# Performance work log

Measured on AMD Instinct MI355X. Metric: run time of the kernel, lower is better.

## Reference

```python
import jax, jax.numpy as jnp
import numpy as np

N_NODES = 100000
N_EDGES = 1600000
N_GRAPHS = 1024
N_FEAT = 128
HID = 64
N_CLASSES = 16
N_CENT = 3  # centroids per class


def setup_inputs() -> dict:
    key = jax.random.key(0)
    ks = jax.random.split(key, 8)
    x = jax.random.normal(ks[0], (N_NODES, N_FEAT), dtype=jnp.float32)
    edge_index = jax.random.randint(ks[1], (2, N_EDGES), 0, N_NODES, dtype=jnp.int64)
    batch = jnp.sort(jax.random.randint(ks[2], (N_NODES,), 0, N_GRAPHS, dtype=jnp.int64))
    s = 1.0 / np.sqrt(N_FEAT)
    W1 = jax.random.normal(ks[3], (N_FEAT, HID), dtype=jnp.float32) * s
    W2 = jax.random.normal(ks[4], (HID, HID), dtype=jnp.float32) * (1.0 / np.sqrt(HID))
    W3 = jax.random.normal(ks[5], (HID, HID), dtype=jnp.float32) * (1.0 / np.sqrt(HID))
    b1 = jnp.zeros((HID,), jnp.float32)
    b2 = jnp.zeros((HID,), jnp.float32)
    b3 = jnp.zeros((HID,), jnp.float32)
    centroids = jax.random.normal(ks[6], (N_CLASSES * N_CENT, HID), dtype=jnp.float32)
    reject_bias = jnp.zeros((1,), jnp.float32)
    return {"x": x, "edge_index": edge_index, "batch": batch,
            "W1": W1, "b1": b1, "W2": W2, "b2": b2, "W3": W3, "b3": b3,
            "centroids": centroids, "reject_bias": reject_bias}


def _gcn_conv(x, W, b, src, dst, norm, n_nodes):
    # PyG GCNConv: out[dst] = sum_e norm_e * (x[src_e] @ W), + bias
    h = x @ W                      # [N, out]
    msg = h[src] * norm[:, None]   # [E+N, out] gather + scale
    out = jax.ops.segment_sum(msg, dst, num_segments=n_nodes)
    return out + b


def reference(x, edge_index, batch, W1, b1, W2, b2, W3, b3, centroids, reject_bias):
    n = x.shape[0]
    loops = jnp.arange(n, dtype=edge_index.dtype)
    src = jnp.concatenate([edge_index[0], loops])
    dst = jnp.concatenate([edge_index[1], loops])
    # symmetric normalization on A + I
    deg = jax.ops.segment_sum(jnp.ones_like(dst, dtype=x.dtype), dst, num_segments=n)
    dinv = jax.lax.rsqrt(jnp.maximum(deg, 1.0))
    norm = dinv[src] * dinv[dst]

    h = jax.nn.relu(_gcn_conv(x, W1, b1, src, dst, norm, n))  # dropout is identity at eval
    h = jax.nn.relu(_gcn_conv(h, W2, b2, src, dst, norm, n))
    h = _gcn_conv(h, W3, b3, src, dst, norm, n)

    # global mean pool over graphs in the batch
    summ = jax.ops.segment_sum(h, batch, num_segments=N_GRAPHS)          # [G, HID]
    cnt = jax.ops.segment_sum(jnp.ones((n,), h.dtype), batch, num_segments=N_GRAPHS)
    emb = summ / jnp.maximum(cnt, 1.0)[:, None]

    # centroid distance head: squared euclidean to all class centroids
    d = (jnp.sum(emb * emb, -1, keepdims=True)
         - 2.0 * emb @ centroids.T
         + jnp.sum(centroids * centroids, -1))                           # [G, 16*3]
    d_pc = jnp.min(d.reshape(-1, N_CLASSES, N_CENT), axis=-1)            # [G, 16]
    class_logits = -d_pc
    reject_logit = jnp.min(d_pc, axis=-1, keepdims=True) - reject_bias   # [G, 1]
    return jnp.concatenate([class_logits, reject_logit], axis=-1)        # [G, 17]
```

## Files before the change

kernel.cpp:

```cpp
#include <hip/hip_runtime.h>

#define HID 64
#define NCLS 16
#define NCENT 3
#define NCENTS (NCLS * NCENT)
#define BSHIFT 9
#define BINW (1 << BSHIFT)
#define NBINMAX 256
#define CHUNK 4096
#define EPT (CHUNK / 256)
#define NU 8

static inline int ceil_div(int a, int b) { return (a + b - 1) / b; }

__device__ inline unsigned short f2bf(float f) {
    unsigned int u = __float_as_uint(f);
    return (unsigned short)((u + 0x7FFFu + ((u >> 16) & 1u)) >> 16);
}
__device__ inline unsigned int pack2bf(float lo, float hi) {
    return (unsigned int)f2bf(lo) | ((unsigned int)f2bf(hi) << 16);
}
__device__ inline float bf2f(unsigned short h) {
    return __uint_as_float(((unsigned int)h) << 16);
}
__device__ inline float bflo(unsigned int u) { return __uint_as_float(u << 16); }
__device__ inline float bfhi(unsigned int u) { return __uint_as_float(u & 0xFFFF0000u); }


__global__ void k_count(const int* __restrict__ dst, int* __restrict__ binCnt,
                        int E, int nbins) {
    __shared__ int c[NBINMAX];
    for (int i = threadIdx.x; i < nbins; i += 256) c[i] = 0;
    __syncthreads();
    int e = blockIdx.x * CHUNK + threadIdx.x;
#pragma unroll
    for (int j = 0; j < EPT; j++, e += 256)
        if (e < E) atomicAdd(&c[dst[e] >> BSHIFT], 1);
    __syncthreads();
    for (int i = threadIdx.x; i < nbins; i += 256)
        if (c[i] > 0) atomicAdd(&binCnt[i], c[i]);
}

__global__ void k_binoff(const int* __restrict__ binCnt, int* __restrict__ binBase,
                         int nbins, int E) {
    __shared__ int ts[NBINMAX];
    int t = threadIdx.x;
    int v = (t < nbins) ? binCnt[t] : 0;
    ts[t] = v;
    __syncthreads();
    for (int off = 1; off < NBINMAX; off <<= 1) {
        int x = (t >= off) ? ts[t - off] : 0;
        __syncthreads();
        ts[t] += x;
        __syncthreads();
    }
    if (t < nbins) binBase[t] = ts[t] - v;
    if (t == 0) binBase[nbins] = E;
}

__global__ __launch_bounds__(256) void k_bin(const int* __restrict__ src,
                                             const int* __restrict__ dst,
                                             const int* __restrict__ binBase,
                                             int* __restrict__ binCur,
                                             int2* __restrict__ binned,
                                             int E, int nbins) {
    __shared__ int cnt[NBINMAX], off[NBINMAX], gbase[NBINMAX];
    __shared__ int2 stage[CHUNK];
    const int c0 = blockIdx.x * CHUNK;
    const int tid = threadIdx.x;
    cnt[tid] = 0;
    __syncthreads();
    int sv[EPT], dv[EPT];
#pragma unroll
    for (int j = 0; j < EPT; j++) {
        int e = c0 + j * 256 + tid;
        dv[j] = -1;
        if (e < E) {
            sv[j] = src[e];
            dv[j] = dst[e];
            atomicAdd(&cnt[dv[j] >> BSHIFT], 1);
        }
    }
    __syncthreads();
    off[tid] = cnt[tid];
    __syncthreads();
    for (int o = 1; o < NBINMAX; o <<= 1) {
        int x = (tid >= o) ? off[tid - o] : 0;
        __syncthreads();
        off[tid] += x;
        __syncthreads();
    }
    int excl = off[tid] - cnt[tid];
    __syncthreads();
    off[tid] = excl;
    gbase[tid] = (tid < nbins && cnt[tid] > 0) ? atomicAdd(&binCur[tid], cnt[tid]) : 0;
    cnt[tid] = 0;
    __syncthreads();
#pragma unroll
    for (int j = 0; j < EPT; j++)
        if (dv[j] >= 0) {
            int b = dv[j] >> BSHIFT;
            int pos = off[b] + atomicAdd(&cnt[b], 1);
            stage[pos] = make_int2(sv[j], dv[j]);
        }
    __syncthreads();
    int tot = min(CHUNK, E - c0);
    for (int i = tid; i < tot; i += 256) {
        int2 v = stage[i];
        int b = v.y >> BSHIFT;
        binned[binBase[b] + gbase[b] + (i - off[b])] = v;
    }
}

__global__ __launch_bounds__(256) void k_fillc2(const int2* __restrict__ binned,
                                                const int* __restrict__ binBase,
                                                int* __restrict__ col,
                                                int* __restrict__ rs_out,
                                                int* __restrict__ deg_out,
                                                float* __restrict__ dinv_out, int N) {
    __shared__ int c[BINW];
    __shared__ int rsl[BINW];
    __shared__ int ts[256];
    int b = blockIdx.x;
    int s = binBase[b], e = binBase[b + 1];
    int n0 = b << BSHIFT;
    int t = threadIdx.x;
    c[2 * t] = 0; c[2 * t + 1] = 0;
    __syncthreads();
    for (int i = s + t; i < e; i += 256)
        atomicAdd(&c[binned[i].y - n0], 1);
    __syncthreads();
    int v0 = c[2 * t], v1 = c[2 * t + 1];
    ts[t] = v0 + v1;
    __syncthreads();
    for (int off = 1; off < 256; off <<= 1) {
        int x = (t >= off) ? ts[t - off] : 0;
        __syncthreads();
        ts[t] += x;
        __syncthreads();
    }
    int base = binBase[b] + ts[t] - (v0 + v1);
    rsl[2 * t] = base;
    rsl[2 * t + 1] = base + v0;
    int n = n0 + 2 * t;
    if (n < N) {
        deg_out[n] = v0; rs_out[n] = base;
        dinv_out[n] = rsqrtf((float)(v0 + 1));
    }
    if (n + 1 < N) {
        deg_out[n + 1] = v1; rs_out[n + 1] = base + v0;
        dinv_out[n + 1] = rsqrtf((float)(v1 + 1));
    }
    c[2 * t] = 0; c[2 * t + 1] = 0;
    __syncthreads();
    for (int i = s + t; i < e; i += 256) {
        int2 v = binned[i];
        int lo = v.y - n0;
        int pos = rsl[lo] + atomicAdd(&c[lo], 1);
        col[pos] = v.x;
    }
}


template <int K, bool BF>
__global__ __launch_bounds__(256) void k_gemm(const void* __restrict__ Ain,
                                              const float* __restrict__ W,
                                              unsigned short* __restrict__ out,
                                              const float* __restrict__ dinv, int N) {
    __shared__ float Ws[64 * HID];
    __shared__ float As[64][68];
    const int tx = threadIdx.x & 15;
    const int ty = threadIdx.x >> 4;
    const int row0 = blockIdx.x * 64;

    float acc[4][4] = {};

    for (int k0 = 0; k0 < K; k0 += 64) {
        if (k0 > 0) __syncthreads();
        for (int i = threadIdx.x; i < 64 * 16; i += 256)
            ((float4*)Ws)[i] = ((const float4*)(W + (size_t)k0 * HID))[i];
        for (int i = threadIdx.x; i < 64 * 16; i += 256) {
            int r = i >> 4, c = i & 15;
            int row = row0 + r;
            float4 v = {0.f, 0.f, 0.f, 0.f};
            if (row < N) {
                if (BF) {
                    ushort4 u = *(const ushort4*)((const unsigned short*)Ain +
                                                  (size_t)row * K + k0 + 4 * c);
                    v.x = bf2f(u.x); v.y = bf2f(u.y); v.z = bf2f(u.z); v.w = bf2f(u.w);
                } else {
                    v = *(const float4*)((const float*)Ain + (size_t)row * K + k0 + 4 * c);
                }
            }
            *(float4*)&As[r][4 * c] = v;
        }
        __syncthreads();
#pragma unroll 4
        for (int k = 0; k < 64; k++) {
            float4 w = *(const float4*)&Ws[k * HID + 4 * tx];
#pragma unroll
            for (int i = 0; i < 4; i++) {
                float a = As[4 * ty + i][k];
                acc[i][0] = fmaf(a, w.x, acc[i][0]);
                acc[i][1] = fmaf(a, w.y, acc[i][1]);
                acc[i][2] = fmaf(a, w.z, acc[i][2]);
                acc[i][3] = fmaf(a, w.w, acc[i][3]);
            }
        }
    }
#pragma unroll
    for (int i = 0; i < 4; i++) {
        int row = row0 + 4 * ty + i;
        if (row < N) {
            float d = dinv[row];
            ushort4 v = {f2bf(d * acc[i][0]), f2bf(d * acc[i][1]),
                         f2bf(d * acc[i][2]), f2bf(d * acc[i][3])};
            *(ushort4*)&out[(size_t)row * HID + 4 * tx] = v;
        }
    }
}


__global__ void k_agg(const unsigned short* __restrict__ tin,
                      unsigned short* __restrict__ out,
                      const int* __restrict__ rs, const int* __restrict__ deg,
                      const int* __restrict__ col,
                      const float* __restrict__ dinv, const float* __restrict__ bias,
                      int N, int relu) {
    int node = (blockIdx.x * blockDim.x + threadIdx.x) >> 3;
    int l = threadIdx.x & 7;
    if (node >= N) return;
    float di = dinv[node];
    uint4 tb = ((const uint4*)(tin + (size_t)node * HID))[l];
    float a0 = bflo(tb.x), a1 = bfhi(tb.x);
    float a2 = bflo(tb.y), a3 = bfhi(tb.y);
    float a4 = bflo(tb.z), a5 = bfhi(tb.z);
    float a6 = bflo(tb.w), a7 = bfhi(tb.w);

    int beg = rs[node];
    int cnt = deg[node];
    int last = beg + cnt - 1;
    for (int e = 0; e < cnt; e += NU) {
        int sv[NU];
#pragma unroll
        for (int j = 0; j < NU; j++) {
            int idx = beg + e + j;
            sv[j] = col[idx < last ? idx : last];
        }
        uint4 vv[NU];
#pragma unroll
        for (int j = 0; j < NU; j++) vv[j] = ((const uint4*)(tin + (size_t)sv[j] * HID))[l];
#pragma unroll
        for (int j = 0; j < NU; j++) {
            a0 += bflo(vv[j].x); a1 += bfhi(vv[j].x);
            a2 += bflo(vv[j].y); a3 += bfhi(vv[j].y);
            a4 += bflo(vv[j].z); a5 += bfhi(vv[j].z);
            a6 += bflo(vv[j].w); a7 += bfhi(vv[j].w);
        }
    }
    int pad = (NU - (cnt & (NU - 1))) & (NU - 1);
    if (cnt > 0 && pad > 0) {
        float fp = (float)pad;
        uint4 vl = ((const uint4*)(tin + (size_t)col[last] * HID))[l];
        a0 = fmaf(-fp, bflo(vl.x), a0); a1 = fmaf(-fp, bfhi(vl.x), a1);
        a2 = fmaf(-fp, bflo(vl.y), a2); a3 = fmaf(-fp, bfhi(vl.y), a3);
        a4 = fmaf(-fp, bflo(vl.z), a4); a5 = fmaf(-fp, bfhi(vl.z), a5);
        a6 = fmaf(-fp, bflo(vl.w), a6); a7 = fmaf(-fp, bfhi(vl.w), a7);
    }
    float4 b0 = ((const float4*)bias)[2 * l];
    float4 b1 = ((const float4*)bias)[2 * l + 1];
    a0 = fmaf(di, a0, b0.x); a1 = fmaf(di, a1, b0.y);
    a2 = fmaf(di, a2, b0.z); a3 = fmaf(di, a3, b0.w);
    a4 = fmaf(di, a4, b1.x); a5 = fmaf(di, a5, b1.y);
    a6 = fmaf(di, a6, b1.z); a7 = fmaf(di, a7, b1.w);
    if (relu) {
        a0 = fmaxf(a0, 0.f); a1 = fmaxf(a1, 0.f); a2 = fmaxf(a2, 0.f); a3 = fmaxf(a3, 0.f);
        a4 = fmaxf(a4, 0.f); a5 = fmaxf(a5, 0.f); a6 = fmaxf(a6, 0.f); a7 = fmaxf(a7, 0.f);
    }
    uint4 o;
    o.x = pack2bf(a0, a1); o.y = pack2bf(a2, a3);
    o.z = pack2bf(a4, a5); o.w = pack2bf(a6, a7);
    ((uint4*)(out + (size_t)node * HID))[l] = o;
}


__global__ void k_pool_head(const unsigned short* __restrict__ h,
                            const int* __restrict__ batch,
                            const float* __restrict__ cent, const float* __restrict__ rbias,
                            float* __restrict__ out, int N) {
    int g = blockIdx.x;
    int lo = 0, hi = N;
    while (lo < hi) { int mid = (lo + hi) >> 1; if (batch[mid] < g) lo = mid + 1; else hi = mid; }
    int s = lo;
    lo = 0; hi = N;
    while (lo < hi) { int mid = (lo + hi) >> 1; if (batch[mid] < g + 1) lo = mid + 1; else hi = mid; }
    int e = lo;

    __shared__ float part[4][HID];
    __shared__ float embS[HID];
    __shared__ float dS[NCENTS];
    __shared__ float dpcS[NCLS];

    int lane = threadIdx.x & 63, wid = threadIdx.x >> 6;
    float acc = 0.0f;
    for (int i = s + wid; i < e; i += 4) acc += bf2f(h[(size_t)i * HID + lane]);
    part[wid][lane] = acc;
    __syncthreads();
    if (wid == 0) {
        float v = part[0][lane] + part[1][lane] + part[2][lane] + part[3][lane];
        embS[lane] = v / fmaxf((float)(e - s), 1.0f);
    }
    __syncthreads();
    if (threadIdx.x < NCENTS) {
        const float* c = cent + threadIdx.x * HID;
        float d = 0.0f;
        for (int k = 0; k < HID; k++) { float df = embS[k] - c[k]; d = fmaf(df, df, d); }
        dS[threadIdx.x] = d;
    }
    __syncthreads();
    if (threadIdx.x < NCLS) {
        float m = fminf(dS[threadIdx.x * 3],
                        fminf(dS[threadIdx.x * 3 + 1], dS[threadIdx.x * 3 + 2]));
        dpcS[threadIdx.x] = m;
        out[g * (NCLS + 1) + threadIdx.x] = -m;
    }
    __syncthreads();
    if (threadIdx.x == 0) {
        float m = dpcS[0];
        for (int i = 1; i < NCLS; i++) m = fminf(m, dpcS[i]);
        out[g * (NCLS + 1) + NCLS] = m - rbias[0];
    }
}


extern "C" void kernel_launch(void* const* d_in, const int* in_sizes, int n_in,
                              void* d_out, int out_size, void* d_ws, size_t ws_size,
                              hipStream_t stream) {
    const float* x    = (const float*)d_in[0];
    const int*   ei   = (const int*)d_in[1];
    const int*   bat  = (const int*)d_in[2];
    const float* W1   = (const float*)d_in[3];
    const float* b1   = (const float*)d_in[4];
    const float* W2   = (const float*)d_in[5];
    const float* b2   = (const float*)d_in[6];
    const float* W3   = (const float*)d_in[7];
    const float* b3   = (const float*)d_in[8];
    const float* cent = (const float*)d_in[9];
    const float* rb   = (const float*)d_in[10];
    float* out = (float*)d_out;

    const int N = in_sizes[0] / 128;
    const int E = in_sizes[1] / 2;
    const int nbins = (N + BINW - 1) >> BSHIFT;

    char* p = (char*)d_ws;
    unsigned short* A  = (unsigned short*)p; p += (size_t)N * HID * 2;
    unsigned short* Bb = (unsigned short*)p; p += (size_t)N * HID * 2;
    int2*  binned = (int2*)p;  p += (size_t)E * 8;
    int*   col    = (int*)p;   p += (size_t)E * 4;
    float* dinv   = (float*)p; p += (size_t)N * 4;
    int*   rs     = (int*)p;   p += (size_t)N * 4;
    int*   deg    = (int*)p;   p += (size_t)N * 4;
    int*   binBase= (int*)p;   p += (NBINMAX + 2) * 4;
    int*   binCnt = (int*)p;   p += NBINMAX * 4;
    int*   binCur = (int*)p;   p += NBINMAX * 4;

    hipMemsetAsync(binCnt, 0, 2 * NBINMAX * 4, stream);

    k_count<<<ceil_div(E, CHUNK), 256, 0, stream>>>(ei + E, binCnt, E, nbins);
    k_binoff<<<1, 256, 0, stream>>>(binCnt, binBase, nbins, E);
    k_bin<<<ceil_div(E, CHUNK), 256, 0, stream>>>(ei, ei + E, binBase, binCur, binned, E, nbins);
    k_fillc2<<<nbins, 256, 0, stream>>>(binned, binBase, col, rs, deg, dinv, N);

    k_gemm<128, false><<<ceil_div(N, 64), 256, 0, stream>>>(x, W1, A, dinv, N);
    k_agg<<<ceil_div(N * 8, 256), 256, 0, stream>>>(A, Bb, rs, deg, col, dinv, b1, N, 1);
    k_gemm<64, true><<<ceil_div(N, 64), 256, 0, stream>>>(Bb, W2, A, dinv, N);
    k_agg<<<ceil_div(N * 8, 256), 256, 0, stream>>>(A, Bb, rs, deg, col, dinv, b2, N, 1);
    k_gemm<64, true><<<ceil_div(N, 64), 256, 0, stream>>>(Bb, W3, A, dinv, N);
    k_agg<<<ceil_div(N * 8, 256), 256, 0, stream>>>(A, Bb, rs, deg, col, dinv, b3, N, 0);

    k_pool_head<<<1024, 256, 0, stream>>>(Bb, bat, cent, rb, out, N);
}
```

Measured before the change: 345.3 us.

## Replace FP32 SIMT GEMMs with split-bf16 MFMA GEMMs and prepacked weights

Swaps the shared-memory FP32 FMA GEMM for a 16x16x32 bf16 MFMA kernel. Weights are split into high and low bf16 parts and pre-swizzled into the MFMA fragment layout by a small prep kernel. The fp32 first-layer input is split the same way, giving three MFMAs per tile to keep near-fp32 accuracy, while the bf16 inputs of later layers use two. This removes the LDS staging and the scalar FMA loops, at the cost of an extra launch and scalar 2-byte output stores.

```diff
diff --git a/kernel.cpp b/kernel.cpp
--- a/kernel.cpp
+++ b/kernel.cpp
@@ -25,6 +25,9 @@
 }
 __device__ inline float bflo(unsigned int u) { return __uint_as_float(u << 16); }
 __device__ inline float bfhi(unsigned int u) { return __uint_as_float(u & 0xFFFF0000u); }
+
+typedef short bf16x8 __attribute__((ext_vector_type(8)));
+typedef float f32x4 __attribute__((ext_vector_type(4)));
 
 
 __global__ void k_count(const int* __restrict__ dst, int* __restrict__ binCnt,
@@ -162,60 +165,85 @@
 }
 
 
+__device__ void wprep_one(const float* __restrict__ W, unsigned short* __restrict__ Wh,
+                          unsigned short* __restrict__ Wl, int K) {
+    for (int idx = threadIdx.x; idx < K * 64; idx += 256) {
+        int k = idx >> 6, colc = idx & 63;
+        float f = W[idx];
+        unsigned short h = f2bf(f);
+        unsigned short lo = f2bf(f - bf2f(h));
+        int kt = k >> 5, kin = k & 31, ct = colc >> 4;
+        int ln = ((kin >> 3) << 4) | (colc & 15);
+        int o = (((kt * 4 + ct) * 64) + ln) * 8 + (kin & 7);
+        Wh[o] = h; Wl[o] = lo;
+    }
+}
+
+__global__ void k_wprep(const float* __restrict__ W1, const float* __restrict__ W2,
+                        const float* __restrict__ W3,
+                        unsigned short* __restrict__ W1h, unsigned short* __restrict__ W1l,
+                        unsigned short* __restrict__ W2h, unsigned short* __restrict__ W2l,
+                        unsigned short* __restrict__ W3h, unsigned short* __restrict__ W3l) {
+    if (blockIdx.x == 0) wprep_one(W1, W1h, W1l, 128);
+    else if (blockIdx.x == 1) wprep_one(W2, W2h, W2l, 64);
+    else wprep_one(W3, W3h, W3l, 64);
+}
+
+
 template <int K, bool BF>
-__global__ __launch_bounds__(256) void k_gemm(const void* __restrict__ Ain,
-                                              const float* __restrict__ W,
-                                              unsigned short* __restrict__ out,
-                                              const float* __restrict__ dinv, int N) {
-    __shared__ float Ws[64 * HID];
-    __shared__ float As[64][68];
-    const int tx = threadIdx.x & 15;
-    const int ty = threadIdx.x >> 4;
-    const int row0 = blockIdx.x * 64;
-
-    float acc[4][4] = {};
-
-    for (int k0 = 0; k0 < K; k0 += 64) {
-        if (k0 > 0) __syncthreads();
-        for (int i = threadIdx.x; i < 64 * 16; i += 256)
-            ((float4*)Ws)[i] = ((const float4*)(W + (size_t)k0 * HID))[i];
-        for (int i = threadIdx.x; i < 64 * 16; i += 256) {
-            int r = i >> 4, c = i & 15;
-            int row = row0 + r;
-            float4 v = {0.f, 0.f, 0.f, 0.f};
-            if (row < N) {
-                if (BF) {
-                    ushort4 u = *(const ushort4*)((const unsigned short*)Ain +
-                                                  (size_t)row * K + k0 + 4 * c);
-                    v.x = bf2f(u.x); v.y = bf2f(u.y); v.z = bf2f(u.z); v.w = bf2f(u.w);
-                } else {
-                    v = *(const float4*)((const float*)Ain + (size_t)row * K + k0 + 4 * c);
-                }
+__global__ __launch_bounds__(256) void k_gemm_mfma(const void* __restrict__ Ain,
+                                                   const unsigned short* __restrict__ Wh,
+                                                   const unsigned short* __restrict__ Wl,
+                                                   unsigned short* __restrict__ out,
+                                                   const float* __restrict__ dinv, int N) {
+    const int lane = threadIdx.x & 63;
+    const int wave = threadIdx.x >> 6;
+    const int row0 = blockIdx.x * 64 + wave * 16;
+    int arow = row0 + (lane & 15);
+    if (arow > N - 1) arow = N - 1;
+    const int kb = (lane >> 4) * 8;
+
+    f32x4 acc[4] = {};
+
+#pragma unroll
+    for (int kt = 0; kt < K / 32; ++kt) {
+        bf16x8 ah, al;
+        if (BF) {
+            ah = *(const bf16x8*)((const unsigned short*)Ain + (size_t)arow * K + kt * 32 + kb);
+        } else {
+            const float* ap = (const float*)Ain + (size_t)arow * K + kt * 32 + kb;
+            float4 f0 = *(const float4*)ap;
+            float4 f1 = *(const float4*)(ap + 4);
+            float fv[8] = {f0.x, f0.y, f0.z, f0.w, f1.x, f1.y, f1.z, f1.w};
+#pragma unroll
+            for (int j = 0; j < 8; ++j) {
+                unsigned short h = f2bf(fv[j]);
+                ah[j] = (short)h;
+                al[j] = (short)f2bf(fv[j] - bf2f(h));
             }
-            *(float4*)&As[r][4 * c] = v;
-        }
-        __syncthreads();
-#pragma unroll 4
-        for (int k = 0; k < 64; k++) {
-            float4 w = *(const float4*)&Ws[k * HID + 4 * tx];
-#pragma unroll
-            for (int i = 0; i < 4; i++) {
-                float a = As[4 * ty + i][k];
-                acc[i][0] = fmaf(a, w.x, acc[i][0]);
-                acc[i][1] = fmaf(a, w.y, acc[i][1]);
-                acc[i][2] = fmaf(a, w.z, acc[i][2]);
-                acc[i][3] = fmaf(a, w.w, acc[i][3]);
-            }
-        }
-    }
-#pragma unroll
-    for (int i = 0; i < 4; i++) {
-        int row = row0 + 4 * ty + i;
+        }
+#pragma unroll
+        for (int ct = 0; ct < 4; ++ct) {
+            const size_t wo = ((size_t)(kt * 4 + ct) * 64 + lane) * 8;
+            bf16x8 wh = *(const bf16x8*)(Wh + wo);
+            bf16x8 wl = *(const bf16x8*)(Wl + wo);
+            acc[ct] = __builtin_amdgcn_mfma_f32_16x16x32_bf16(ah, wh, acc[ct], 0, 0, 0);
+            if (!BF)
+                acc[ct] = __builtin_amdgcn_mfma_f32_16x16x32_bf16(al, wh, acc[ct], 0, 0, 0);
+            acc[ct] = __builtin_amdgcn_mfma_f32_16x16x32_bf16(ah, wl, acc[ct], 0, 0, 0);
+        }
+    }
+
+    const int rb = row0 + (lane >> 4) * 4;
+    const int cb = lane & 15;
+#pragma unroll
+    for (int i = 0; i < 4; ++i) {
+        int row = rb + i;
         if (row < N) {
             float d = dinv[row];
-            ushort4 v = {f2bf(d * acc[i][0]), f2bf(d * acc[i][1]),
-                         f2bf(d * acc[i][2]), f2bf(d * acc[i][3])};
-            *(ushort4*)&out[(size_t)row * HID + 4 * tx] = v;
+#pragma unroll
+            for (int ct = 0; ct < 4; ++ct)
+                out[(size_t)row * HID + ct * 16 + cb] = f2bf(d * acc[ct][i]);
         }
     }
 }
@@ -364,19 +392,28 @@
     int*   binBase= (int*)p;   p += (NBINMAX + 2) * 4;
     int*   binCnt = (int*)p;   p += NBINMAX * 4;
     int*   binCur = (int*)p;   p += NBINMAX * 4;
+    p = (char*)(((uintptr_t)p + 15) & ~(uintptr_t)15);
+    unsigned short* W1h = (unsigned short*)p; p += 8192 * 2;
+    unsigned short* W1l = (unsigned short*)p; p += 8192 * 2;
+    unsigned short* W2h = (unsigned short*)p; p += 4096 * 2;
+    unsigned short* W2l = (unsigned short*)p; p += 4096 * 2;
+    unsigned short* W3h = (unsigned short*)p; p += 4096 * 2;
+    unsigned short* W3l = (unsigned short*)p; p += 4096 * 2;
 
     hipMemsetAsync(binCnt, 0, 2 * NBINMAX * 4, stream);
+
+    k_wprep<<<3, 256, 0, stream>>>(W1, W2, W3, W1h, W1l, W2h, W2l, W3h, W3l);
 
     k_count<<<ceil_div(E, CHUNK), 256, 0, stream>>>(ei + E, binCnt, E, nbins);
     k_binoff<<<1, 256, 0, stream>>>(binCnt, binBase, nbins, E);
     k_bin<<<ceil_div(E, CHUNK), 256, 0, stream>>>(ei, ei + E, binBase, binCur, binned, E, nbins);
     k_fillc2<<<nbins, 256, 0, stream>>>(binned, binBase, col, rs, deg, dinv, N);
 
-    k_gemm<128, false><<<ceil_div(N, 64), 256, 0, stream>>>(x, W1, A, dinv, N);
+    k_gemm_mfma<128, false><<<ceil_div(N, 64), 256, 0, stream>>>(x, W1h, W1l, A, dinv, N);
     k_agg<<<ceil_div(N * 8, 256), 256, 0, stream>>>(A, Bb, rs, deg, col, dinv, b1, N, 1);
-    k_gemm<64, true><<<ceil_div(N, 64), 256, 0, stream>>>(Bb, W2, A, dinv, N);
+    k_gemm_mfma<64, true><<<ceil_div(N, 64), 256, 0, stream>>>(Bb, W2h, W2l, A, dinv, N);
     k_agg<<<ceil_div(N * 8, 256), 256, 0, stream>>>(A, Bb, rs, deg, col, dinv, b2, N, 1);
-    k_gemm<64, true><<<ceil_div(N, 64), 256, 0, stream>>>(Bb, W3, A, dinv, N);
+    k_gemm_mfma<64, true><<<ceil_div(N, 64), 256, 0, stream>>>(Bb, W3h, W3l, A, dinv, N);
     k_agg<<<ceil_div(N * 8, 256), 256, 0, stream>>>(A, Bb, rs, deg, col, dinv, b3, N, 0);
 
     k_pool_head<<<1024, 256, 0, stream>>>(Bb, bat, cent, rb, out, N);
```

After: 331.5 us. -4.0%, faster.
